# Optimization experiments

Measured on AMD Instinct MI355X. Metric: run time of the kernel, lower is better.

Reference implementation:

```python
import jax, jax.numpy as jnp
import numpy as np

N, T, F, HID, HEADS, E = 10000, 6, 64, 64, 4, 160000


def gat_conv(x, W, a_src, a_dst, bias, src, dst, n, concat):
    """PyG-style GATConv (self-loops already appended to src/dst).
    x: [n, in]; W: [in, H*C]; a_src/a_dst: [H, C]; returns ([n, H*C] or [n, C], alpha [E', H])."""
    H, C = a_src.shape
    xw = (x @ W).reshape(n, H, C)
    # per-edge unnormalized attention logits
    al = (xw * a_src).sum(-1)[src] + (xw * a_dst).sum(-1)[dst]  # [E', H]
    al = jax.nn.leaky_relu(al, 0.2)
    # segment softmax over destination neighborhoods
    m = jax.ops.segment_max(al, dst, num_segments=n)
    ex = jnp.exp(al - m[dst])
    s = jax.ops.segment_sum(ex, dst, num_segments=n)
    alpha = ex / (s[dst] + 1e-16)
    out = jax.ops.segment_sum(xw[src] * alpha[:, :, None], dst, num_segments=n)  # [n, H, C]
    out = out.reshape(n, H * C) if concat else out.mean(axis=1)
    return out + bias, alpha


def setup_inputs() -> dict:
    key = jax.random.key(0)
    ks = jax.random.split(key, 12)
    sc = 0.05
    return {
        "x": jax.random.normal(ks[0], (N, T, F), jnp.float32),
        "edge_index": jax.random.randint(ks[1], (2, E), 0, N, jnp.int64),
        "W0": jax.random.normal(ks[2], (F, HID), jnp.float32) * sc,
        "a_src0": jax.random.normal(ks[3], (HEADS, HID // HEADS), jnp.float32) * sc,
        "a_dst0": jax.random.normal(ks[4], (HEADS, HID // HEADS), jnp.float32) * sc,
        "b0": jnp.zeros((HID,), jnp.float32),
        "W1": jax.random.normal(ks[5], (HID, HEADS * HID), jnp.float32) * sc,
        "a_src1": jax.random.normal(ks[6], (HEADS, HID), jnp.float32) * sc,
        "a_dst1": jax.random.normal(ks[7], (HEADS, HID), jnp.float32) * sc,
        "b1": jnp.zeros((HID,), jnp.float32),
        "ln_g": jnp.ones((HID,), jnp.float32),
        "ln_b": jnp.zeros((HID,), jnp.float32),
        "W_ih": jax.random.normal(ks[8], (3 * HID, HID), jnp.float32) * sc,
        "W_hh": jax.random.normal(ks[9], (3 * HID, HID), jnp.float32) * sc,
        "b_ih": jnp.zeros((3 * HID,), jnp.float32),
        "b_hh": jnp.zeros((3 * HID,), jnp.float32),
    }


def reference(x, edge_index, W0, a_src0, a_dst0, b0, W1, a_src1, a_dst1, b1,
              ln_g, ln_b, W_ih, W_hh, b_ih, b_hh):
    n = x.shape[0]
    loops = jnp.arange(n)
    src = jnp.concatenate([edge_index[0], loops])  # add self loops
    dst = jnp.concatenate([edge_index[1], loops])

    def gat_step(_, xt):
        h, _a = gat_conv(xt, W0, a_src0, a_dst0, b0, src, dst, n, True)
        h = jax.nn.elu(h)  # dropout is identity in eval mode
        h, alpha = gat_conv(h, W1, a_src1, a_dst1, b1, src, dst, n, False)
        h = jax.nn.elu(h)
        mu = h.mean(-1, keepdims=True)
        v = ((h - mu) ** 2).mean(-1, keepdims=True)
        h = (h - mu) / jnp.sqrt(v + 1e-5) * ln_g + ln_b
        return None, (h, alpha)

    _, (Hs, alphas) = jax.lax.scan(gat_step, None, jnp.moveaxis(x, 1, 0))  # Hs: [T, n, HID]

    def gru_step(h, xt):
        gi = xt @ W_ih.T + b_ih
        gh = h @ W_hh.T + b_hh
        ir, iz, ig = jnp.split(gi, 3, axis=-1)
        hr, hz, hg = jnp.split(gh, 3, axis=-1)
        r = jax.nn.sigmoid(ir + hr)
        z = jax.nn.sigmoid(iz + hz)
        g = jnp.tanh(ig + r * hg)
        return (1.0 - z) * g + z * h, None

    h0 = jnp.zeros((n, W_hh.shape[1]), x.dtype)
    hT, _ = jax.lax.scan(gru_step, h0, Hs)  # last GRU output == last hidden (1 layer)
    attn_edge_index = jnp.stack([src, dst])
    return hT, alphas[-1], attn_edge_index
```

## Files before the change

### kernel.cpp

```cpp
#include <hip/hip_runtime.h>
#include <hip/hip_bf16.h>
#include <cstdint>
#include <cstddef>

#define N_NODES 10000
#define T_STEPS 6
#define F_IN    64
#define HID     64
#define HEADS   4
#define E_EDGES 160000
#define EP      (E_EDGES + N_NODES)
#define TN      (T_STEPS * N_NODES)
#define NTILES  (TN / 16)

typedef __hip_bfloat16 bf16;
typedef __attribute__((ext_vector_type(8))) short short8;
typedef __attribute__((ext_vector_type(4))) float floatx4;

__device__ __forceinline__ float bfu(unsigned short s) { return __uint_as_float((unsigned)s << 16); }
__device__ __forceinline__ unsigned short f2bu(float f) {
    bf16 b = __float2bfloat16(f);
    return *(unsigned short*)&b;
}
__device__ __forceinline__ void lds_fence() {
    asm volatile("s_waitcnt lgkmcnt(0)" ::: "memory");
}


__global__ void k_count(const int* ei, int* counts) {
    int e = blockIdx.x * blockDim.x + threadIdx.x;
    if (e >= EP) return;
    int dst = (e < E_EDGES) ? ei[E_EDGES + e] : (e - E_EDGES);
    atomicAdd(&counts[dst], 1);
}

__global__ void k_scan(const int* counts, int* rowstart) {
    __shared__ int part[1024];
    int tid = threadIdx.x;
    const int chunk = (N_NODES + 1023) / 1024;
    int base = tid * chunk;
    int s = 0;
    for (int i = 0; i < chunk; i++) { int idx = base + i; if (idx < N_NODES) s += counts[idx]; }
    part[tid] = s;
    __syncthreads();
    for (int off = 1; off < 1024; off <<= 1) {
        int v = (tid >= off) ? part[tid - off] : 0;
        __syncthreads();
        part[tid] += v;
        __syncthreads();
    }
    int run = (tid == 0) ? 0 : part[tid - 1];
    for (int i = 0; i < chunk; i++) {
        int idx = base + i;
        if (idx < N_NODES) { rowstart[idx] = run; run += counts[idx]; }
    }
    if (tid == 0) rowstart[N_NODES] = EP;
}

__global__ void k_scatter(const int* ei, const int* rowstart, int* fill,
                          int* csr_src, int* csr_eid, float* out_ei) {
    int e = blockIdx.x * blockDim.x + threadIdx.x;
    if (e >= EP) return;
    int src = (e < E_EDGES) ? ei[e] : (e - E_EDGES);
    int dst = (e < E_EDGES) ? ei[E_EDGES + e] : (e - E_EDGES);
    int pos = rowstart[dst] + atomicAdd(&fill[dst], 1);
    csr_src[pos] = src;
    csr_eid[pos] = e;
    out_ei[e] = (float)src;
    out_ei[EP + e] = (float)dst;
}


__global__ __launch_bounds__(256) void k_prep(const float* __restrict__ W0,
                                              const float* __restrict__ W1,
                                              const float* __restrict__ a_src0,
                                              const float* __restrict__ a_dst0,
                                              const float* __restrict__ a_src1,
                                              const float* __restrict__ a_dst1,
                                              const float* __restrict__ W_ih,
                                              const float* __restrict__ W_hh,
                                              bf16* __restrict__ W0bt,
                                              bf16* __restrict__ W1bt,
                                              bf16* __restrict__ wihb,
                                              bf16* __restrict__ whhb,
                                              float* __restrict__ P0s,
                                              float* __restrict__ P0d,
                                              float* __restrict__ P1s,
                                              float* __restrict__ P1d) {
    int b = blockIdx.x, tid = threadIdx.x;
    if (b == 176) {
        int h = tid >> 6, k = tid & 63;
        float ps = 0.f, pd = 0.f;
        for (int c = 0; c < 64; c++) {
            float wv = W1[k * 256 + h * 64 + c];
            ps += wv * a_src1[h * 64 + c];
            pd += wv * a_dst1[h * 64 + c];
        }
        P1s[h * 64 + k] = ps;
        P1d[h * 64 + k] = pd;
        return;
    }
    if (b == 177) {
        int h = tid >> 6, k = tid & 63;
        float ps = 0.f, pd = 0.f;
        for (int c = 0; c < 16; c++) {
            float wv = W0[k * 64 + h * 16 + c];
            ps += wv * a_src0[h * 16 + c];
            pd += wv * a_dst0[h * 16 + c];
        }
        P0s[h * 64 + k] = ps;
        P0d[h * 64 + k] = pd;
        return;
    }
    int i = b * 256 + tid;
    if (i < 4096) {
        W0bt[i] = __float2bfloat16(W0[(i & 63) * 64 + (i >> 6)]);
    } else if (i < 20480) {
        int j = i - 4096; int c = j >> 8, K = j & 255;
        W1bt[j] = __float2bfloat16(W1[(K & 63) * 256 + (K >> 6) * 64 + c]);
    } else if (i < 32768) {
        wihb[i - 20480] = __float2bfloat16(W_ih[i - 20480]);
    } else {
        whhb[i - 32768] = __float2bfloat16(W_hh[i - 32768]);
    }
}

__global__ __launch_bounds__(256) void k_gemm0(const float* __restrict__ x,
                                               const bf16* __restrict__ W0bt,
                                               const float* __restrict__ P0s,
                                               const float* __restrict__ P0d,
                                               bf16* __restrict__ XW0b,
                                               float* __restrict__ ALS0,
                                               float* __restrict__ ALD0) {
    __shared__ __align__(16) bf16 wt[64 * 64];
    int tid = threadIdx.x;
    for (int i = tid; i < 512; i += 256)
        ((short8*)wt)[i] = ((const short8*)W0bt)[i];
    __syncthreads();
    int wv = tid >> 6, lane = tid & 63;
    int tile = blockIdx.x * 4 + wv;
    if (tile >= NTILES) return;
    int rb = tile * 16;
    int m = lane & 15, quad = lane >> 4;
    int row = rb + m;
    int t = row / N_NODES, n = row - t * N_NODES;
    const float* xr = x + ((size_t)n * T_STEPS + t) * F_IN + quad * 8;
    short8 a0, a1;
#pragma unroll
    for (int j = 0; j < 8; j++) {
        a0[j] = (short)f2bu(xr[j]);
        a1[j] = (short)f2bu(xr[32 + j]);
    }
    floatx4 acc[4];
#pragma unroll
    for (int ct = 0; ct < 4; ct++) {
        short8 bb0 = *(const short8*)(wt + (ct * 16 + m) * 64 + quad * 8);
        short8 bb1 = *(const short8*)(wt + (ct * 16 + m) * 64 + 32 + quad * 8);
        floatx4 a = {0.f, 0.f, 0.f, 0.f};
        a = __builtin_amdgcn_mfma_f32_16x16x32_bf16(a0, bb0, a, 0, 0, 0);
        a = __builtin_amdgcn_mfma_f32_16x16x32_bf16(a1, bb1, a, 0, 0, 0);
        acc[ct] = a;
    }
    short8 p0, p1;
#pragma unroll
    for (int j = 0; j < 8; j++) {
        int k0 = quad * 8 + j, k1 = 32 + quad * 8 + j;
        float v0 = 0.f, v1 = 0.f;
        if (m < 4)      { v0 = P0s[m * 64 + k0];       v1 = P0s[m * 64 + k1]; }
        else if (m < 8) { v0 = P0d[(m - 4) * 64 + k0]; v1 = P0d[(m - 4) * 64 + k1]; }
        p0[j] = (short)f2bu(v0);
        p1[j] = (short)f2bu(v1);
    }
    floatx4 ac5 = {0.f, 0.f, 0.f, 0.f};
    ac5 = __builtin_amdgcn_mfma_f32_16x16x32_bf16(a0, p0, ac5, 0, 0, 0);
    ac5 = __builtin_amdgcn_mfma_f32_16x16x32_bf16(a1, p1, ac5, 0, 0, 0);
#pragma unroll
    for (int ct = 0; ct < 4; ct++)
#pragma unroll
        for (int r = 0; r < 4; r++)
            XW0b[(size_t)(rb + quad * 4 + r) * 64 + ct * 16 + m] = __float2bfloat16(acc[ct][r]);
#pragma unroll
    for (int r = 0; r < 4; r++) {
        int orow = rb + quad * 4 + r;
        if (m < 4)      ALS0[orow * 4 + m] = ac5[r];
        else if (m < 8) ALD0[orow * 4 + (m - 4)] = ac5[r];
    }
}

__global__ __launch_bounds__(256) void k_fused0(const int* __restrict__ rowst,
                                                const int* __restrict__ csr_src,
                                                const bf16* __restrict__ XW0b,
                                                const float* __restrict__ ALS0,
                                                const float* __restrict__ ALD0,
                                                const float* __restrict__ b0,
                                                bf16* __restrict__ H0b) {
    __shared__ float exv[4][4][65][4];
    __shared__ int   srcs[4][4][68];
    int tid = threadIdx.x;
    int wv = tid >> 6, lane = tid & 63;
    int sub = lane >> 4, il = lane & 15;
    int wid = (blockIdx.x * 4 + wv) * 4 + sub;
    int t = wid / N_NODES, n = wid - t * N_NODES;
    int rs = rowst[n], re = rowst[n + 1];
    int deg = re - rs;
    int tb = t * N_NODES;
    int hsel = il >> 2;
    float4 ad = *(const float4*)(ALD0 + (size_t)wid * 4);
    float s0 = 0.f, s1 = 0.f, s2 = 0.f, s3 = 0.f;
    float a0 = 0.f, a1 = 0.f, a2 = 0.f, a3 = 0.f;
    float i0, i1, i2, i3;
    const bf16* hrow = XW0b + (size_t)tb * 64 + il * 4;

    if (deg <= 64) {
        for (int b = 0; b < deg; b += 16) {
            int idx = b + il;
            bool valid = idx < deg;
            int src = csr_src[valid ? (rs + idx) : rs];
            float4 as = *(const float4*)(ALS0 + (size_t)(tb + src) * 4);
            float l0 = as.x + ad.x; l0 = l0 > 0.f ? l0 : 0.2f * l0;
            float l1 = as.y + ad.y; l1 = l1 > 0.f ? l1 : 0.2f * l1;
            float l2 = as.z + ad.z; l2 = l2 > 0.f ? l2 : 0.2f * l2;
            float l3 = as.w + ad.w; l3 = l3 > 0.f ? l3 : 0.2f * l3;
            float e0 = valid ? __expf(fminf(l0, 80.f)) : 0.f;
            float e1 = valid ? __expf(fminf(l1, 80.f)) : 0.f;
            float e2 = valid ? __expf(fminf(l2, 80.f)) : 0.f;
            float e3 = valid ? __expf(fminf(l3, 80.f)) : 0.f;
            s0 += e0; s1 += e1; s2 += e2; s3 += e3;
            float4 ex4; ex4.x = e0; ex4.y = e1; ex4.z = e2; ex4.w = e3;
            *(float4*)&exv[wv][sub][idx][0] = ex4;
            srcs[wv][sub][idx] = src;
        }
#pragma unroll
        for (int o = 1; o <= 8; o <<= 1) {
            s0 += __shfl_xor(s0, o, 64); s1 += __shfl_xor(s1, o, 64);
            s2 += __shfl_xor(s2, o, 64); s3 += __shfl_xor(s3, o, 64);
        }
        i0 = 1.f / (s0 + 1e-16f); i1 = 1.f / (s1 + 1e-16f);
        i2 = 1.f / (s2 + 1e-16f); i3 = 1.f / (s3 + 1e-16f);
        lds_fence();
        for (int k = 0; k < deg; k++) {
            float aex = exv[wv][sub][k][hsel];
            int sx = srcs[wv][sub][k];
            ushort4 u = *(const ushort4*)(hrow + sx * 64);
            a0 += aex * bfu(u.x); a1 += aex * bfu(u.y);
            a2 += aex * bfu(u.z); a3 += aex * bfu(u.w);
        }
    } else {
        for (int idx = il; idx < deg; idx += 16) {
            int src = csr_src[rs + idx];
            float4 as = *(const float4*)(ALS0 + (size_t)(tb + src) * 4);
            float l0 = as.x + ad.x; l0 = l0 > 0.f ? l0 : 0.2f * l0; s0 += __expf(fminf(l0, 80.f));
            float l1 = as.y + ad.y; l1 = l1 > 0.f ? l1 : 0.2f * l1; s1 += __expf(fminf(l1, 80.f));
            float l2 = as.z + ad.z; l2 = l2 > 0.f ? l2 : 0.2f * l2; s2 += __expf(fminf(l2, 80.f));
            float l3 = as.w + ad.w; l3 = l3 > 0.f ? l3 : 0.2f * l3; s3 += __expf(fminf(l3, 80.f));
        }
#pragma unroll
        for (int o = 1; o <= 8; o <<= 1) {
            s0 += __shfl_xor(s0, o, 64); s1 += __shfl_xor(s1, o, 64);
            s2 += __shfl_xor(s2, o, 64); s3 += __shfl_xor(s3, o, 64);
        }
        i0 = 1.f / (s0 + 1e-16f); i1 = 1.f / (s1 + 1e-16f);
        i2 = 1.f / (s2 + 1e-16f); i3 = 1.f / (s3 + 1e-16f);
        for (int cb = 0; cb < deg; cb += 64) {
            int cend = min(64, deg - cb);
            lds_fence();
            for (int q = 0; q < 64; q += 16) {
                int idx = q + il;
                bool valid = idx < cend;
                int src = csr_src[valid ? (rs + cb + idx) : rs];
                float4 as = *(const float4*)(ALS0 + (size_t)(tb + src) * 4);
                float l0 = as.x + ad.x; l0 = l0 > 0.f ? l0 : 0.2f * l0;
                float l1 = as.y + ad.y; l1 = l1 > 0.f ? l1 : 0.2f * l1;
                float l2 = as.z + ad.z; l2 = l2 > 0.f ? l2 : 0.2f * l2;
                float l3 = as.w + ad.w; l3 = l3 > 0.f ? l3 : 0.2f * l3;
                float4 ex4;
                ex4.x = valid ? __expf(fminf(l0, 80.f)) : 0.f;
                ex4.y = valid ? __expf(fminf(l1, 80.f)) : 0.f;
                ex4.z = valid ? __expf(fminf(l2, 80.f)) : 0.f;
                ex4.w = valid ? __expf(fminf(l3, 80.f)) : 0.f;
                *(float4*)&exv[wv][sub][idx][0] = ex4;
                srcs[wv][sub][idx] = src;
            }
            lds_fence();
            for (int k = 0; k < cend; k++) {
                float aex = exv[wv][sub][k][hsel];
                int sx = srcs[wv][sub][k];
                ushort4 u = *(const ushort4*)(hrow + sx * 64);
                a0 += aex * bfu(u.x); a1 += aex * bfu(u.y);
                a2 += aex * bfu(u.z); a3 += aex * bfu(u.w);
            }
        }
    }
    float ih = (hsel == 0) ? i0 : (hsel == 1) ? i1 : (hsel == 2) ? i2 : i3;
    float4 bv = *(const float4*)(b0 + il * 4);
    float v0 = a0 * ih + bv.x; v0 = v0 > 0.f ? v0 : (__expf(v0) - 1.f);
    float v1 = a1 * ih + bv.y; v1 = v1 > 0.f ? v1 : (__expf(v1) - 1.f);
    float v2 = a2 * ih + bv.z; v2 = v2 > 0.f ? v2 : (__expf(v2) - 1.f);
    float v3 = a3 * ih + bv.w; v3 = v3 > 0.f ? v3 : (__expf(v3) - 1.f);
    ushort4 o4;
    o4.x = f2bu(v0); o4.y = f2bu(v1); o4.z = f2bu(v2); o4.w = f2bu(v3);
    *(ushort4*)(H0b + (size_t)wid * 64 + il * 4) = o4;
}

__global__ __launch_bounds__(256) void k_logits1(const bf16* __restrict__ H0b,
                                                 const float* __restrict__ P1s,
                                                 const float* __restrict__ P1d,
                                                 float* __restrict__ ALS1,
                                                 float* __restrict__ ALD1) {
    int tid = threadIdx.x;
    int wv = tid >> 6, lane = tid & 63;
    int tile = blockIdx.x * 4 + wv;
    if (tile >= NTILES) return;
    int rb = tile * 16;
    int m = lane & 15, quad = lane >> 4;
    short8 a0 = *(const short8*)(H0b + (size_t)(rb + m) * 64 + quad * 8);
    short8 a1 = *(const short8*)(H0b + (size_t)(rb + m) * 64 + 32 + quad * 8);
    short8 bb0, bb1;
#pragma unroll
    for (int j = 0; j < 8; j++) {
        int k0 = quad * 8 + j, k1 = 32 + quad * 8 + j;
        float v0 = 0.f, v1 = 0.f;
        if (m < 4)      { v0 = P1s[m * 64 + k0];       v1 = P1s[m * 64 + k1]; }
        else if (m < 8) { v0 = P1d[(m - 4) * 64 + k0]; v1 = P1d[(m - 4) * 64 + k1]; }
        bb0[j] = (short)f2bu(v0);
        bb1[j] = (short)f2bu(v1);
    }
    floatx4 acc = {0.f, 0.f, 0.f, 0.f};
    acc = __builtin_amdgcn_mfma_f32_16x16x32_bf16(a0, bb0, acc, 0, 0, 0);
    acc = __builtin_amdgcn_mfma_f32_16x16x32_bf16(a1, bb1, acc, 0, 0, 0);
#pragma unroll
    for (int r = 0; r < 4; r++) {
        int row = rb + quad * 4 + r;
        if (m < 4)      ALS1[row * 4 + m] = acc[r];
        else if (m < 8) ALD1[row * 4 + (m - 4)] = acc[r];
    }
}

__global__ __launch_bounds__(256) void k_fused1(const int* __restrict__ rowst,
                                                const int* __restrict__ csr_src,
                                                const int* __restrict__ csr_eid,
                                                const bf16* __restrict__ H0b,
                                                const float* __restrict__ ALS1,
                                                const float* __restrict__ ALD1,
                                                bf16* __restrict__ AGG1b,
                                                float* __restrict__ out_alpha) {
    __shared__ float exv[4][4][65][4];
    __shared__ int   srcs[4][4][68];
    int tid = threadIdx.x;
    int wv = tid >> 6, lane = tid & 63;
    int sub = lane >> 4, il = lane & 15;
    int wid = (blockIdx.x * 4 + wv) * 4 + sub;
    int t = wid / N_NODES, n = wid - t * N_NODES;
    int rs = rowst[n], re = rowst[n + 1];
    int deg = re - rs;
    int tb = t * N_NODES;
    bool do_out = (t == T_STEPS - 1);
    float4 ad = *(const float4*)(ALD1 + (size_t)wid * 4);
    float s0 = 0.f, s1 = 0.f, s2 = 0.f, s3 = 0.f;
    float acc[4][4];
#pragma unroll
    for (int hh = 0; hh < 4; hh++)
#pragma unroll
        for (int j = 0; j < 4; j++) acc[hh][j] = 0.f;
    float i0, i1, i2, i3;
    const bf16* hrow = H0b + (size_t)tb * 64 + il * 4;

    if (deg <= 64) {
        for (int b = 0; b < deg; b += 16) {
            int idx = b + il;
            bool valid = idx < deg;
            int src = csr_src[valid ? (rs + idx) : rs];
            float4 as = *(const float4*)(ALS1 + (size_t)(tb + src) * 4);
            float l0 = as.x + ad.x; l0 = l0 > 0.f ? l0 : 0.2f * l0;
            float l1 = as.y + ad.y; l1 = l1 > 0.f ? l1 : 0.2f * l1;
            float l2 = as.z + ad.z; l2 = l2 > 0.f ? l2 : 0.2f * l2;
            float l3 = as.w + ad.w; l3 = l3 > 0.f ? l3 : 0.2f * l3;
            float e0 = valid ? __expf(fminf(l0, 80.f)) : 0.f;
            float e1 = valid ? __expf(fminf(l1, 80.f)) : 0.f;
            float e2 = valid ? __expf(fminf(l2, 80.f)) : 0.f;
            float e3 = valid ? __expf(fminf(l3, 80.f)) : 0.f;
            s0 += e0; s1 += e1; s2 += e2; s3 += e3;
            float4 ex4; ex4.x = e0; ex4.y = e1; ex4.z = e2; ex4.w = e3;
            *(float4*)&exv[wv][sub][idx][0] = ex4;
            srcs[wv][sub][idx] = src;
        }
#pragma unroll
        for (int o = 1; o <= 8; o <<= 1) {
            s0 += __shfl_xor(s0, o, 64); s1 += __shfl_xor(s1, o, 64);
            s2 += __shfl_xor(s2, o, 64); s3 += __shfl_xor(s3, o, 64);
        }
        i0 = 1.f / (s0 + 1e-16f); i1 = 1.f / (s1 + 1e-16f);
        i2 = 1.f / (s2 + 1e-16f); i3 = 1.f / (s3 + 1e-16f);
        lds_fence();
        if (do_out) {
            for (int b = 0; b < deg; b += 16) {
                int idx = b + il;
                if (idx < deg) {
                    int eid = csr_eid[rs + idx];
                    float4 ex4 = *(const float4*)&exv[wv][sub][idx][0];
                    float4 o4;
                    o4.x = ex4.x * i0; o4.y = ex4.y * i1;
                    o4.z = ex4.z * i2; o4.w = ex4.w * i3;
                    *(float4*)(out_alpha + (size_t)eid * 4) = o4;
                }
            }
        }
        for (int k = 0; k < deg; k++) {
            float4 ex = *(const float4*)&exv[wv][sub][k][0];
            int sx = srcs[wv][sub][k];
            ushort4 u = *(const ushort4*)(hrow + sx * 64);
            float x0 = bfu(u.x), x1 = bfu(u.y), x2 = bfu(u.z), x3 = bfu(u.w);
            acc[0][0] += ex.x * x0; acc[0][1] += ex.x * x1; acc[0][2] += ex.x * x2; acc[0][3] += ex.x * x3;
            acc[1][0] += ex.y * x0; acc[1][1] += ex.y * x1; acc[1][2] += ex.y * x2; acc[1][3] += ex.y * x3;
            acc[2][0] += ex.z * x0; acc[2][1] += ex.z * x1; acc[2][2] += ex.z * x2; acc[2][3] += ex.z * x3;
            acc[3][0] += ex.w * x0; acc[3][1] += ex.w * x1; acc[3][2] += ex.w * x2; acc[3][3] += ex.w * x3;
        }
    } else {
        for (int idx = il; idx < deg; idx += 16) {
            int src = csr_src[rs + idx];
            float4 as = *(const float4*)(ALS1 + (size_t)(tb + src) * 4);
            float l0 = as.x + ad.x; l0 = l0 > 0.f ? l0 : 0.2f * l0; s0 += __expf(fminf(l0, 80.f));
            float l1 = as.y + ad.y; l1 = l1 > 0.f ? l1 : 0.2f * l1; s1 += __expf(fminf(l1, 80.f));
            float l2 = as.z + ad.z; l2 = l2 > 0.f ? l2 : 0.2f * l2; s2 += __expf(fminf(l2, 80.f));
            float l3 = as.w + ad.w; l3 = l3 > 0.f ? l3 : 0.2f * l3; s3 += __expf(fminf(l3, 80.f));
        }
#pragma unroll
        for (int o = 1; o <= 8; o <<= 1) {
            s0 += __shfl_xor(s0, o, 64); s1 += __shfl_xor(s1, o, 64);
            s2 += __shfl_xor(s2, o, 64); s3 += __shfl_xor(s3, o, 64);
        }
        i0 = 1.f / (s0 + 1e-16f); i1 = 1.f / (s1 + 1e-16f);
        i2 = 1.f / (s2 + 1e-16f); i3 = 1.f / (s3 + 1e-16f);
        for (int cb = 0; cb < deg; cb += 64) {
            int cend = min(64, deg - cb);
            lds_fence();
            for (int q = 0; q < 64; q += 16) {
                int idx = q + il;
                bool valid = idx < cend;
                int e = rs + cb + idx;
                int src = csr_src[valid ? e : rs];
                float4 as = *(const float4*)(ALS1 + (size_t)(tb + src) * 4);
                float l0 = as.x + ad.x; l0 = l0 > 0.f ? l0 : 0.2f * l0;
                float l1 = as.y + ad.y; l1 = l1 > 0.f ? l1 : 0.2f * l1;
                float l2 = as.z + ad.z; l2 = l2 > 0.f ? l2 : 0.2f * l2;
                float l3 = as.w + ad.w; l3 = l3 > 0.f ? l3 : 0.2f * l3;
                float e0 = valid ? __expf(fminf(l0, 80.f)) : 0.f;
                float e1 = valid ? __expf(fminf(l1, 80.f)) : 0.f;
                float e2 = valid ? __expf(fminf(l2, 80.f)) : 0.f;
                float e3 = valid ? __expf(fminf(l3, 80.f)) : 0.f;
                float4 ex4; ex4.x = e0; ex4.y = e1; ex4.z = e2; ex4.w = e3;
                *(float4*)&exv[wv][sub][idx][0] = ex4;
                srcs[wv][sub][idx] = src;
                if (do_out && valid) {
                    int eid = csr_eid[e];
                    float4 o4;
                    o4.x = e0 * i0; o4.y = e1 * i1; o4.z = e2 * i2; o4.w = e3 * i3;
                    *(float4*)(out_alpha + (size_t)eid * 4) = o4;
                }
            }
            lds_fence();
            for (int k = 0; k < cend; k++) {
                float4 ex = *(const float4*)&exv[wv][sub][k][0];
                int sx = srcs[wv][sub][k];
                ushort4 u = *(const ushort4*)(hrow + sx * 64);
                float x0 = bfu(u.x), x1 = bfu(u.y), x2 = bfu(u.z), x3 = bfu(u.w);
                acc[0][0] += ex.x * x0; acc[0][1] += ex.x * x1; acc[0][2] += ex.x * x2; acc[0][3] += ex.x * x3;
                acc[1][0] += ex.y * x0; acc[1][1] += ex.y * x1; acc[1][2] += ex.y * x2; acc[1][3] += ex.y * x3;
                acc[2][0] += ex.z * x0; acc[2][1] += ex.z * x1; acc[2][2] += ex.z * x2; acc[2][3] += ex.z * x3;
                acc[3][0] += ex.w * x0; acc[3][1] += ex.w * x1; acc[3][2] += ex.w * x2; acc[3][3] += ex.w * x3;
            }
        }
    }
    float iv[4] = { i0, i1, i2, i3 };
    int ob = wid * 256 + il * 4;
#pragma unroll
    for (int hh = 0; hh < 4; hh++) {
        ushort4 o4;
        o4.x = f2bu(acc[hh][0] * iv[hh]); o4.y = f2bu(acc[hh][1] * iv[hh]);
        o4.z = f2bu(acc[hh][2] * iv[hh]); o4.w = f2bu(acc[hh][3] * iv[hh]);
        *(ushort4*)(AGG1b + (size_t)ob + hh * 64) = o4;
    }
}

__global__ __launch_bounds__(256) void k_post1(const bf16* __restrict__ AGG1b,
                                               const bf16* __restrict__ W1bt,
                                               const float* __restrict__ b1,
                                               const float* __restrict__ ln_g,
                                               const float* __restrict__ ln_b,
                                               bf16* __restrict__ HSb) {
    __shared__ __align__(16) bf16 wt[64 * 256];
    int tid = threadIdx.x;
    for (int i = tid; i < 2048; i += 256)
        ((short8*)wt)[i] = ((const short8*)W1bt)[i];
    __syncthreads();
    int wv = tid >> 6, lane = tid & 63;
    int tile = blockIdx.x * 4 + wv;
    if (tile >= NTILES) return;
    int rb = tile * 16;
    int m = lane & 15, quad = lane >> 4;
    const bf16* arow = AGG1b + (size_t)(rb + m) * 256 + quad * 8;
    short8 af[8];
#pragma unroll
    for (int kb = 0; kb < 8; kb++) af[kb] = *(const short8*)(arow + kb * 32);
    floatx4 acc[4];
#pragma unroll
    for (int ct = 0; ct < 4; ct++) {
        const bf16* wrow = wt + (ct * 16 + m) * 256 + quad * 8;
        floatx4 a = {0.f, 0.f, 0.f, 0.f};
#pragma unroll
        for (int kb = 0; kb < 8; kb++) {
            short8 bf = *(const short8*)(wrow + kb * 32);
            a = __builtin_amdgcn_mfma_f32_16x16x32_bf16(af[kb], bf, a, 0, 0, 0);
        }
        acc[ct] = a;
    }
    float b1v[4], ggv[4], bbv[4];
#pragma unroll
    for (int ct = 0; ct < 4; ct++) {
        b1v[ct] = b1[ct * 16 + m]; ggv[ct] = ln_g[ct * 16 + m]; bbv[ct] = ln_b[ct * 16 + m];
    }
#pragma unroll
    for (int r = 0; r < 4; r++) {
        float v[4];
        float s = 0.f;
#pragma unroll
        for (int ct = 0; ct < 4; ct++) {
            float t_ = acc[ct][r] * 0.25f + b1v[ct];
            t_ = t_ > 0.f ? t_ : (__expf(t_) - 1.f);
            v[ct] = t_; s += t_;
        }
#pragma unroll
        for (int o = 8; o; o >>= 1) s += __shfl_xor(s, o, 64);
        float mu = s * (1.f / 64.f);
        float q = 0.f;
#pragma unroll
        for (int ct = 0; ct < 4; ct++) { float d = v[ct] - mu; q += d * d; }
#pragma unroll
        for (int o = 8; o; o >>= 1) q += __shfl_xor(q, o, 64);
        float rinv = rsqrtf(q * (1.f / 64.f) + 1e-5f);
        int row = rb + quad * 4 + r;
#pragma unroll
        for (int ct = 0; ct < 4; ct++)
            HSb[(size_t)row * 64 + ct * 16 + m] =
                __float2bfloat16((v[ct] - mu) * rinv * ggv[ct] + bbv[ct]);
    }
}

__global__ __launch_bounds__(256) void k_gru(const bf16* __restrict__ HSb,
                                             const bf16* __restrict__ wihb,
                                             const float* __restrict__ b_ih,
                                             const bf16* __restrict__ whhb,
                                             const float* __restrict__ b_hh,
                                             float* __restrict__ outh) {
    __shared__ __align__(16) bf16 hbuf[16 * 72];
    int tid = threadIdx.x;
    int wv = tid >> 6, lane = tid & 63;
    int rb = blockIdx.x * 16;
    int m = lane & 15, quad = lane >> 4;
    int fb = wv * 16;
    const int rowR = (fb + m) * 64, rowZ = (64 + fb + m) * 64, rowG = (128 + fb + m) * 64;
    short8 Br0 = *(const short8*)(wihb + rowR + quad * 8);
    short8 Br1 = *(const short8*)(wihb + rowR + 32 + quad * 8);
    short8 Bz0 = *(const short8*)(wihb + rowZ + quad * 8);
    short8 Bz1 = *(const short8*)(wihb + rowZ + 32 + quad * 8);
    short8 Bg0 = *(const short8*)(wihb + rowG + quad * 8);
    short8 Bg1 = *(const short8*)(wihb + rowG + 32 + quad * 8);
    short8 Cr0 = *(const short8*)(whhb + rowR + quad * 8);
    short8 Cr1 = *(const short8*)(whhb + rowR + 32 + quad * 8);
    short8 Cz0 = *(const short8*)(whhb + rowZ + quad * 8);
    short8 Cz1 = *(const short8*)(whhb + rowZ + 32 + quad * 8);
    short8 Cg0 = *(const short8*)(whhb + rowG + quad * 8);
    short8 Cg1 = *(const short8*)(whhb + rowG + 32 + quad * 8);
    float biR = b_ih[fb + m], biZ = b_ih[64 + fb + m], biG = b_ih[128 + fb + m];
    float bhR = b_hh[fb + m], bhZ = b_hh[64 + fb + m], bhG = b_hh[128 + fb + m];
    float hprev[4] = {0.f, 0.f, 0.f, 0.f};

    for (int t = 0; t < T_STEPS; t++) {
        const bf16* xr = HSb + ((size_t)t * N_NODES + rb + m) * 64;
        short8 ax0 = *(const short8*)(xr + quad * 8);
        short8 ax1 = *(const short8*)(xr + 32 + quad * 8);
        short8 ah0, ah1;
        if (t > 0) {
            ah0 = *(const short8*)(hbuf + m * 72 + quad * 8);
            ah1 = *(const short8*)(hbuf + m * 72 + 32 + quad * 8);
        }
        __syncthreads();
        floatx4 aR = {0.f, 0.f, 0.f, 0.f}, aZ = {0.f, 0.f, 0.f, 0.f};
        floatx4 aGi = {0.f, 0.f, 0.f, 0.f}, aGh = {0.f, 0.f, 0.f, 0.f};
        aR = __builtin_amdgcn_mfma_f32_16x16x32_bf16(ax0, Br0, aR, 0, 0, 0);
        aR = __builtin_amdgcn_mfma_f32_16x16x32_bf16(ax1, Br1, aR, 0, 0, 0);
        aZ = __builtin_amdgcn_mfma_f32_16x16x32_bf16(ax0, Bz0, aZ, 0, 0, 0);
        aZ = __builtin_amdgcn_mfma_f32_16x16x32_bf16(ax1, Bz1, aZ, 0, 0, 0);
        aGi = __builtin_amdgcn_mfma_f32_16x16x32_bf16(ax0, Bg0, aGi, 0, 0, 0);
        aGi = __builtin_amdgcn_mfma_f32_16x16x32_bf16(ax1, Bg1, aGi, 0, 0, 0);
        if (t > 0) {
            aR = __builtin_amdgcn_mfma_f32_16x16x32_bf16(ah0, Cr0, aR, 0, 0, 0);
            aR = __builtin_amdgcn_mfma_f32_16x16x32_bf16(ah1, Cr1, aR, 0, 0, 0);
            aZ = __builtin_amdgcn_mfma_f32_16x16x32_bf16(ah0, Cz0, aZ, 0, 0, 0);
            aZ = __builtin_amdgcn_mfma_f32_16x16x32_bf16(ah1, Cz1, aZ, 0, 0, 0);
            aGh = __builtin_amdgcn_mfma_f32_16x16x32_bf16(ah0, Cg0, aGh, 0, 0, 0);
            aGh = __builtin_amdgcn_mfma_f32_16x16x32_bf16(ah1, Cg1, aGh, 0, 0, 0);
        }
#pragma unroll
        for (int r = 0; r < 4; r++) {
            float rr = 1.f / (1.f + __expf(-(aR[r] + biR + bhR)));
            float z  = 1.f / (1.f + __expf(-(aZ[r] + biZ + bhZ)));
            float g  = tanhf(aGi[r] + biG + rr * (aGh[r] + bhG));
            hprev[r] = (1.f - z) * g + z * hprev[r];
        }
        if (t < T_STEPS - 1) {
#pragma unroll
            for (int r = 0; r < 4; r++)
                hbuf[(quad * 4 + r) * 72 + fb + m] = __float2bfloat16(hprev[r]);
            __syncthreads();
        }
    }
#pragma unroll
    for (int r = 0; r < 4; r++)
        outh[(size_t)(rb + quad * 4 + r) * 64 + fb + m] = hprev[r];
}


extern "C" void kernel_launch(void* const* d_in, const int* in_sizes, int n_in,
                              void* d_out, int out_size, void* d_ws, size_t ws_size,
                              hipStream_t stream) {
    const float* x      = (const float*)d_in[0];
    const int*   ei     = (const int*)d_in[1];
    const float* W0     = (const float*)d_in[2];
    const float* a_src0 = (const float*)d_in[3];
    const float* a_dst0 = (const float*)d_in[4];
    const float* b0     = (const float*)d_in[5];
    const float* W1     = (const float*)d_in[6];
    const float* a_src1 = (const float*)d_in[7];
    const float* a_dst1 = (const float*)d_in[8];
    const float* b1     = (const float*)d_in[9];
    const float* ln_g   = (const float*)d_in[10];
    const float* ln_b   = (const float*)d_in[11];
    const float* W_ih   = (const float*)d_in[12];
    const float* W_hh   = (const float*)d_in[13];
    const float* b_ih   = (const float*)d_in[14];
    const float* b_hh   = (const float*)d_in[15];
    float* out = (float*)d_out;

    char* w = (char*)d_ws;
    size_t off = 0;
    auto take = [&](size_t bytes) -> void* {
        void* p = w + off;
        off = (off + bytes + 255) & ~(size_t)255;
        return p;
    };
    int*   counts  = (int*)take(N_NODES * 4);
    int*   fill    = (int*)take(N_NODES * 4);
    int*   rowst   = (int*)take((N_NODES + 1) * 4);
    int*   csr_src = (int*)take((size_t)EP * 4);
    int*   csr_eid = (int*)take((size_t)EP * 4);
    bf16*  XW0b    = (bf16*)take((size_t)TN * 64 * 2);
    float* ALS0    = (float*)take((size_t)TN * 4 * 4);
    float* ALD0    = (float*)take((size_t)TN * 4 * 4);
    bf16*  H0b     = (bf16*)take((size_t)TN * 64 * 2);
    float* P0s     = (float*)take(256 * 4);
    float* P0d     = (float*)take(256 * 4);
    float* P1s     = (float*)take(256 * 4);
    float* P1d     = (float*)take(256 * 4);
    float* ALS1    = (float*)take((size_t)TN * 4 * 4);
    float* ALD1    = (float*)take((size_t)TN * 4 * 4);
    bf16*  AGG1b   = (bf16*)take((size_t)TN * 256 * 2);
    bf16*  HSb     = (bf16*)take((size_t)TN * 64 * 2);
    bf16*  W0bt    = (bf16*)take(4096 * 2);
    bf16*  W1bt    = (bf16*)take(16384 * 2);
    bf16*  wihb    = (bf16*)take(12288 * 2);
    bf16*  whhb    = (bf16*)take(12288 * 2);
    (void)ws_size; (void)in_sizes; (void)n_in; (void)out_size;

    const int B = 256;
    float* out_ei = out + (size_t)N_NODES * HID + (size_t)EP * HEADS;

    hipMemsetAsync(counts, 0, N_NODES * 4, stream);
    hipMemsetAsync(fill, 0, N_NODES * 4, stream);
    k_count<<<(EP + B - 1) / B, B, 0, stream>>>(ei, counts);
    k_scan<<<1, 1024, 0, stream>>>(counts, rowst);
    k_scatter<<<(EP + B - 1) / B, B, 0, stream>>>(ei, rowst, fill, csr_src, csr_eid, out_ei);
    k_prep<<<178, B, 0, stream>>>(W0, W1, a_src0, a_dst0, a_src1, a_dst1, W_ih, W_hh,
                                  W0bt, W1bt, wihb, whhb, P0s, P0d, P1s, P1d);

    const int GT = (NTILES + 3) / 4;
    k_gemm0<<<GT, B, 0, stream>>>(x, W0bt, P0s, P0d, XW0b, ALS0, ALD0);
    k_fused0<<<TN / 16, B, 0, stream>>>(rowst, csr_src, XW0b, ALS0, ALD0, b0, H0b);
    k_logits1<<<GT, B, 0, stream>>>(H0b, P1s, P1d, ALS1, ALD1);

    k_fused1<<<TN / 16, B, 0, stream>>>(rowst, csr_src, csr_eid, H0b, ALS1, ALD1,
                                        AGG1b, out + (size_t)N_NODES * HID);
    k_post1<<<GT, B, 0, stream>>>(AGG1b, W1bt, b1, ln_g, ln_b, HSb);

    k_gru<<<N_NODES / 16, B, 0, stream>>>(HSb, wihb, b_ih, whhb, b_hh, out);
}
```

Baseline: 228.4 us.

## Fuse layer-1 logits into fused0 and post-projection/LayerNorm into fused1

The layer-1 attention logits are now computed at the end of k_fused0 with per-lane dot products and shuffle reductions, instead of in a separate MFMA kernel. The W1 projection, ELU and LayerNorm are folded into k_fused1 through a shared-memory union, so the large bf16 AGG1 intermediate is no longer written to or read from global memory. The two memsets become one. This removes two launches and a lot of global traffic. In exchange it adds block-wide syncs to a divergent gather kernel, and every block now reads W1 from global memory instead of staging it in LDS.

```diff
diff --git a/kernel.cpp b/kernel.cpp
--- a/kernel.cpp
+++ b/kernel.cpp
@@ -193,7 +193,11 @@
                                                 const float* __restrict__ ALS0,
                                                 const float* __restrict__ ALD0,
                                                 const float* __restrict__ b0,
-                                                bf16* __restrict__ H0b) {
+                                                const float* __restrict__ P1s,
+                                                const float* __restrict__ P1d,
+                                                bf16* __restrict__ H0b,
+                                                float* __restrict__ ALS1,
+                                                float* __restrict__ ALD1) {
     __shared__ float exv[4][4][65][4];
     __shared__ int   srcs[4][4][68];
     int tid = threadIdx.x;
@@ -300,39 +304,28 @@
     ushort4 o4;
     o4.x = f2bu(v0); o4.y = f2bu(v1); o4.z = f2bu(v2); o4.w = f2bu(v3);
     *(ushort4*)(H0b + (size_t)wid * 64 + il * 4) = o4;
-}
-
-__global__ __launch_bounds__(256) void k_logits1(const bf16* __restrict__ H0b,
-                                                 const float* __restrict__ P1s,
-                                                 const float* __restrict__ P1d,
-                                                 float* __restrict__ ALS1,
-                                                 float* __restrict__ ALD1) {
-    int tid = threadIdx.x;
-    int wv = tid >> 6, lane = tid & 63;
-    int tile = blockIdx.x * 4 + wv;
-    if (tile >= NTILES) return;
-    int rb = tile * 16;
-    int m = lane & 15, quad = lane >> 4;
-    short8 a0 = *(const short8*)(H0b + (size_t)(rb + m) * 64 + quad * 8);
-    short8 a1 = *(const short8*)(H0b + (size_t)(rb + m) * 64 + 32 + quad * 8);
-    short8 bb0, bb1;
-#pragma unroll
-    for (int j = 0; j < 8; j++) {
-        int k0 = quad * 8 + j, k1 = 32 + quad * 8 + j;
-        float v0 = 0.f, v1 = 0.f;
-        if (m < 4)      { v0 = P1s[m * 64 + k0];       v1 = P1s[m * 64 + k1]; }
-        else if (m < 8) { v0 = P1d[(m - 4) * 64 + k0]; v1 = P1d[(m - 4) * 64 + k1]; }
-        bb0[j] = (short)f2bu(v0);
-        bb1[j] = (short)f2bu(v1);
-    }
-    floatx4 acc = {0.f, 0.f, 0.f, 0.f};
-    acc = __builtin_amdgcn_mfma_f32_16x16x32_bf16(a0, bb0, acc, 0, 0, 0);
-    acc = __builtin_amdgcn_mfma_f32_16x16x32_bf16(a1, bb1, acc, 0, 0, 0);
-#pragma unroll
-    for (int r = 0; r < 4; r++) {
-        int row = rb + quad * 4 + r;
-        if (m < 4)      ALS1[row * 4 + m] = acc[r];
-        else if (m < 8) ALD1[row * 4 + (m - 4)] = acc[r];
+
+    float ps[4], pd[4];
+#pragma unroll
+    for (int h = 0; h < 4; h++) {
+        float4 s4 = *(const float4*)(P1s + h * 64 + il * 4);
+        float4 d4 = *(const float4*)(P1d + h * 64 + il * 4);
+        ps[h] = v0 * s4.x + v1 * s4.y + v2 * s4.z + v3 * s4.w;
+        pd[h] = v0 * d4.x + v1 * d4.y + v2 * d4.z + v3 * d4.w;
+    }
+#pragma unroll
+    for (int o = 1; o <= 8; o <<= 1) {
+#pragma unroll
+        for (int h = 0; h < 4; h++) {
+            ps[h] += __shfl_xor(ps[h], o, 64);
+            pd[h] += __shfl_xor(pd[h], o, 64);
+        }
+    }
+    if (il == 0) {
+        float4 w1; w1.x = ps[0]; w1.y = ps[1]; w1.z = ps[2]; w1.w = ps[3];
+        *(float4*)(ALS1 + (size_t)wid * 4) = w1;
+        float4 w2; w2.x = pd[0]; w2.y = pd[1]; w2.z = pd[2]; w2.w = pd[3];
+        *(float4*)(ALD1 + (size_t)wid * 4) = w2;
     }
 }
 
@@ -342,10 +335,16 @@
                                                 const bf16* __restrict__ H0b,
                                                 const float* __restrict__ ALS1,
                                                 const float* __restrict__ ALD1,
-                                                bf16* __restrict__ AGG1b,
+                                                const bf16* __restrict__ W1bt,
+                                                const float* __restrict__ b1,
+                                                const float* __restrict__ ln_g,
+                                                const float* __restrict__ ln_b,
+                                                bf16* __restrict__ HSb,
                                                 float* __restrict__ out_alpha) {
-    __shared__ float exv[4][4][65][4];
-    __shared__ int   srcs[4][4][68];
+    __shared__ __align__(16) union SM {
+        struct { float exv[4][4][65][4]; int srcs[4][4][68]; } p;
+        struct { bf16 ast[16][264]; float ost[16][68]; } q;
+    } sm;
     int tid = threadIdx.x;
     int wv = tid >> 6, lane = tid & 63;
     int sub = lane >> 4, il = lane & 15;
@@ -381,8 +380,8 @@
             float e3 = valid ? __expf(fminf(l3, 80.f)) : 0.f;
             s0 += e0; s1 += e1; s2 += e2; s3 += e3;
             float4 ex4; ex4.x = e0; ex4.y = e1; ex4.z = e2; ex4.w = e3;
-            *(float4*)&exv[wv][sub][idx][0] = ex4;
-            srcs[wv][sub][idx] = src;
+            *(float4*)&sm.p.exv[wv][sub][idx][0] = ex4;
+            sm.p.srcs[wv][sub][idx] = src;
         }
 #pragma unroll
         for (int o = 1; o <= 8; o <<= 1) {
@@ -397,7 +396,7 @@
                 int idx = b + il;
                 if (idx < deg) {
                     int eid = csr_eid[rs + idx];
-                    float4 ex4 = *(const float4*)&exv[wv][sub][idx][0];
+                    float4 ex4 = *(const float4*)&sm.p.exv[wv][sub][idx][0];
                     float4 o4;
                     o4.x = ex4.x * i0; o4.y = ex4.y * i1;
                     o4.z = ex4.z * i2; o4.w = ex4.w * i3;
@@ -406,8 +405,8 @@
             }
         }
         for (int k = 0; k < deg; k++) {
-            float4 ex = *(const float4*)&exv[wv][sub][k][0];
-            int sx = srcs[wv][sub][k];
+            float4 ex = *(const float4*)&sm.p.exv[wv][sub][k][0];
+            int sx = sm.p.srcs[wv][sub][k];
             ushort4 u = *(const ushort4*)(hrow + sx * 64);
             float x0 = bfu(u.x), x1 = bfu(u.y), x2 = bfu(u.z), x3 = bfu(u.w);
             acc[0][0] += ex.x * x0; acc[0][1] += ex.x * x1; acc[0][2] += ex.x * x2; acc[0][3] += ex.x * x3;
@@ -449,8 +448,8 @@
                 float e2 = valid ? __expf(fminf(l2, 80.f)) : 0.f;
                 float e3 = valid ? __expf(fminf(l3, 80.f)) : 0.f;
                 float4 ex4; ex4.x = e0; ex4.y = e1; ex4.z = e2; ex4.w = e3;
-                *(float4*)&exv[wv][sub][idx][0] = ex4;
-                srcs[wv][sub][idx] = src;
+                *(float4*)&sm.p.exv[wv][sub][idx][0] = ex4;
+                sm.p.srcs[wv][sub][idx] = src;
                 if (do_out && valid) {
                     int eid = csr_eid[e];
                     float4 o4;
@@ -460,8 +459,8 @@
             }
             lds_fence();
             for (int k = 0; k < cend; k++) {
-                float4 ex = *(const float4*)&exv[wv][sub][k][0];
-                int sx = srcs[wv][sub][k];
+                float4 ex = *(const float4*)&sm.p.exv[wv][sub][k][0];
+                int sx = sm.p.srcs[wv][sub][k];
                 ushort4 u = *(const ushort4*)(hrow + sx * 64);
                 float x0 = bfu(u.x), x1 = bfu(u.y), x2 = bfu(u.z), x3 = bfu(u.w);
                 acc[0][0] += ex.x * x0; acc[0][1] += ex.x * x1; acc[0][2] += ex.x * x2; acc[0][3] += ex.x * x3;
@@ -472,78 +471,54 @@
         }
     }
     float iv[4] = { i0, i1, i2, i3 };
-    int ob = wid * 256 + il * 4;
+
+    __syncthreads();
+    int r_local = wv * 4 + sub;
 #pragma unroll
     for (int hh = 0; hh < 4; hh++) {
         ushort4 o4;
         o4.x = f2bu(acc[hh][0] * iv[hh]); o4.y = f2bu(acc[hh][1] * iv[hh]);
         o4.z = f2bu(acc[hh][2] * iv[hh]); o4.w = f2bu(acc[hh][3] * iv[hh]);
-        *(ushort4*)(AGG1b + (size_t)ob + hh * 64) = o4;
-    }
-}
-
-__global__ __launch_bounds__(256) void k_post1(const bf16* __restrict__ AGG1b,
-                                               const bf16* __restrict__ W1bt,
-                                               const float* __restrict__ b1,
-                                               const float* __restrict__ ln_g,
-                                               const float* __restrict__ ln_b,
-                                               bf16* __restrict__ HSb) {
-    __shared__ __align__(16) bf16 wt[64 * 256];
-    int tid = threadIdx.x;
-    for (int i = tid; i < 2048; i += 256)
-        ((short8*)wt)[i] = ((const short8*)W1bt)[i];
+        *(ushort4*)&sm.q.ast[r_local][hh * 64 + il * 4] = o4;
+    }
     __syncthreads();
-    int wv = tid >> 6, lane = tid & 63;
-    int tile = blockIdx.x * 4 + wv;
-    if (tile >= NTILES) return;
-    int rb = tile * 16;
-    int m = lane & 15, quad = lane >> 4;
-    const bf16* arow = AGG1b + (size_t)(rb + m) * 256 + quad * 8;
-    short8 af[8];
-#pragma unroll
-    for (int kb = 0; kb < 8; kb++) af[kb] = *(const short8*)(arow + kb * 32);
-    floatx4 acc[4];
-#pragma unroll
-    for (int ct = 0; ct < 4; ct++) {
-        const bf16* wrow = wt + (ct * 16 + m) * 256 + quad * 8;
-        floatx4 a = {0.f, 0.f, 0.f, 0.f};
-#pragma unroll
-        for (int kb = 0; kb < 8; kb++) {
-            short8 bf = *(const short8*)(wrow + kb * 32);
-            a = __builtin_amdgcn_mfma_f32_16x16x32_bf16(af[kb], bf, a, 0, 0, 0);
-        }
-        acc[ct] = a;
-    }
-    float b1v[4], ggv[4], bbv[4];
-#pragma unroll
-    for (int ct = 0; ct < 4; ct++) {
-        b1v[ct] = b1[ct * 16 + m]; ggv[ct] = ln_g[ct * 16 + m]; bbv[ct] = ln_b[ct * 16 + m];
-    }
-#pragma unroll
-    for (int r = 0; r < 4; r++) {
-        float v[4];
-        float s = 0.f;
-#pragma unroll
-        for (int ct = 0; ct < 4; ct++) {
-            float t_ = acc[ct][r] * 0.25f + b1v[ct];
-            t_ = t_ > 0.f ? t_ : (__expf(t_) - 1.f);
-            v[ct] = t_; s += t_;
-        }
-#pragma unroll
-        for (int o = 8; o; o >>= 1) s += __shfl_xor(s, o, 64);
-        float mu = s * (1.f / 64.f);
-        float q = 0.f;
-#pragma unroll
-        for (int ct = 0; ct < 4; ct++) { float d = v[ct] - mu; q += d * d; }
-#pragma unroll
-        for (int o = 8; o; o >>= 1) q += __shfl_xor(q, o, 64);
-        float rinv = rsqrtf(q * (1.f / 64.f) + 1e-5f);
-        int row = rb + quad * 4 + r;
-#pragma unroll
-        for (int ct = 0; ct < 4; ct++)
-            HSb[(size_t)row * 64 + ct * 16 + m] =
-                __float2bfloat16((v[ct] - mu) * rinv * ggv[ct] + bbv[ct]);
-    }
+    int m = il, quad = sub;
+    floatx4 ga = {0.f, 0.f, 0.f, 0.f};
+    const bf16* wrow = W1bt + (size_t)(wv * 16 + m) * 256 + quad * 8;
+#pragma unroll
+    for (int kb = 0; kb < 8; kb++) {
+        short8 afk = *(const short8*)&sm.q.ast[m][kb * 32 + quad * 8];
+        short8 bfk = *(const short8*)(wrow + kb * 32);
+        ga = __builtin_amdgcn_mfma_f32_16x16x32_bf16(afk, bfk, ga, 0, 0, 0);
+    }
+#pragma unroll
+    for (int r = 0; r < 4; r++)
+        sm.q.ost[quad * 4 + r][wv * 16 + m] = ga[r];
+    __syncthreads();
+    int row = wv * 4 + quad;
+    float4 vv = *(const float4*)&sm.q.ost[row][m * 4];
+    float4 bb = *(const float4*)(b1 + m * 4);
+    float v0 = vv.x * 0.25f + bb.x; v0 = v0 > 0.f ? v0 : (__expf(v0) - 1.f);
+    float v1 = vv.y * 0.25f + bb.y; v1 = v1 > 0.f ? v1 : (__expf(v1) - 1.f);
+    float v2 = vv.z * 0.25f + bb.z; v2 = v2 > 0.f ? v2 : (__expf(v2) - 1.f);
+    float v3 = vv.w * 0.25f + bb.w; v3 = v3 > 0.f ? v3 : (__expf(v3) - 1.f);
+    float s = v0 + v1 + v2 + v3;
+#pragma unroll
+    for (int o = 1; o <= 8; o <<= 1) s += __shfl_xor(s, o, 64);
+    float mu = s * (1.f / 64.f);
+    float d0 = v0 - mu, d1 = v1 - mu, d2 = v2 - mu, d3 = v3 - mu;
+    float qv = d0 * d0 + d1 * d1 + d2 * d2 + d3 * d3;
+#pragma unroll
+    for (int o = 1; o <= 8; o <<= 1) qv += __shfl_xor(qv, o, 64);
+    float rinv = rsqrtf(qv * (1.f / 64.f) + 1e-5f);
+    float4 gg = *(const float4*)(ln_g + m * 4);
+    float4 lb = *(const float4*)(ln_b + m * 4);
+    ushort4 ho;
+    ho.x = f2bu(d0 * rinv * gg.x + lb.x);
+    ho.y = f2bu(d1 * rinv * gg.y + lb.y);
+    ho.z = f2bu(d2 * rinv * gg.z + lb.z);
+    ho.w = f2bu(d3 * rinv * gg.w + lb.w);
+    *(ushort4*)(HSb + (size_t)(blockIdx.x * 16 + row) * 64 + m * 4) = ho;
 }
 
 __global__ __launch_bounds__(256) void k_gru(const bf16* __restrict__ HSb,
@@ -651,6 +626,7 @@
     };
     int*   counts  = (int*)take(N_NODES * 4);
     int*   fill    = (int*)take(N_NODES * 4);
+    size_t zero_bytes = off;
     int*   rowst   = (int*)take((N_NODES + 1) * 4);
     int*   csr_src = (int*)take((size_t)EP * 4);
     int*   csr_eid = (int*)take((size_t)EP * 4);
@@ -664,7 +640,6 @@
     float* P1d     = (float*)take(256 * 4);
     float* ALS1    = (float*)take((size_t)TN * 4 * 4);
     float* ALD1    = (float*)take((size_t)TN * 4 * 4);
-    bf16*  AGG1b   = (bf16*)take((size_t)TN * 256 * 2);
     bf16*  HSb     = (bf16*)take((size_t)TN * 64 * 2);
     bf16*  W0bt    = (bf16*)take(4096 * 2);
     bf16*  W1bt    = (bf16*)take(16384 * 2);
@@ -675,8 +650,7 @@
     const int B = 256;
     float* out_ei = out + (size_t)N_NODES * HID + (size_t)EP * HEADS;
 
-    hipMemsetAsync(counts, 0, N_NODES * 4, stream);
-    hipMemsetAsync(fill, 0, N_NODES * 4, stream);
+    hipMemsetAsync(counts, 0, zero_bytes, stream);
     k_count<<<(EP + B - 1) / B, B, 0, stream>>>(ei, counts);
     k_scan<<<1, 1024, 0, stream>>>(counts, rowst);
     k_scatter<<<(EP + B - 1) / B, B, 0, stream>>>(ei, rowst, fill, csr_src, csr_eid, out_ei);
@@ -685,12 +659,12 @@
 
     const int GT = (NTILES + 3) / 4;
     k_gemm0<<<GT, B, 0, stream>>>(x, W0bt, P0s, P0d, XW0b, ALS0, ALD0);
-    k_fused0<<<TN / 16, B, 0, stream>>>(rowst, csr_src, XW0b, ALS0, ALD0, b0, H0b);
-    k_logits1<<<GT, B, 0, stream>>>(H0b, P1s, P1d, ALS1, ALD1);
+    k_fused0<<<TN / 16, B, 0, stream>>>(rowst, csr_src, XW0b, ALS0, ALD0, b0,
+                                        P1s, P1d, H0b, ALS1, ALD1);
 
     k_fused1<<<TN / 16, B, 0, stream>>>(rowst, csr_src, csr_eid, H0b, ALS1, ALD1,
-                                        AGG1b, out + (size_t)N_NODES * HID);
-    k_post1<<<GT, B, 0, stream>>>(AGG1b, W1bt, b1, ln_g, ln_b, HSb);
+                                        W1bt, b1, ln_g, ln_b, HSb,
+                                        out + (size_t)N_NODES * HID);
 
     k_gru<<<N_NODES / 16, B, 0, stream>>>(HSb, wihb, b_ih, whhb, b_hh, out);
 }
```

Measured after the change: 225.5 us. About the same (-1.2%).
